# Optimization experiments

Hardware: AMD Instinct MI355X
Metric: run time of the kernel (lower is better)

## Reference

```python
import jax, jax.numpy as jnp
import numpy as np
from jax import lax

T, LC = 4096, 20           # sentence length, max word length in chars
CV, CE, CO = 100, 25, 25   # char vocab, char emb dim, char-cnn out channels
V, E = 100000, 512         # word vocab, word emb dim
H = 1024                   # lstm hidden size per direction
NT, START, STOP = 12, 10, 11
NEG = -10000.0


def _lstm_dir(x, w_ih, w_hh, b_ih, b_hh):
    # x: [T, In] -> hs: [T, H]; pytorch gate order i, f, g, o
    pre = x @ w_ih.T + (b_ih + b_hh)              # [T, 4H] (input part hoisted out of scan)
    h0 = jnp.zeros((H,), x.dtype)
    def step(carry, p):
        h, c = carry
        g = p + h @ w_hh.T
        i, f, gg, o = jnp.split(g, 4)
        i = jax.nn.sigmoid(i); f = jax.nn.sigmoid(f)
        gg = jnp.tanh(gg); o = jax.nn.sigmoid(o)
        c = f * c + i * gg
        h = o * jnp.tanh(c)
        return (h, c), h
    _, hs = lax.scan(step, (h0, h0), pre)
    return hs


def _features(sentence, chars, char_emb, cnn_w, cnn_b, word_emb,
              w_ih_f, w_hh_f, b_ih_f, b_hh_f, w_ih_b, w_hh_b, b_ih_b, b_hh_b,
              w_tag, b_tag):
    # char CNN: embed -> conv2d(kernel (3,CE), pad (2,0)) -> max-pool over full time axis
    ce = char_emb[chars][:, None, :, :]            # [T,1,LC,CE]
    y = lax.conv_general_dilated(ce, cnn_w, (1, 1), ((2, 2), (0, 0)),
                                 dimension_numbers=('NCHW', 'OIHW', 'NCHW'))
    y = y + cnn_b[None, :, None, None]             # [T,CO,LC+2,1]
    char_feat = y.max(axis=(2, 3))                 # [T,CO]
    emb = jnp.concatenate([word_emb[sentence], char_feat], axis=1)  # [T,E+CO]
    # dropout is identity in eval mode
    hf = _lstm_dir(emb, w_ih_f, w_hh_f, b_ih_f, b_hh_f)
    hb = _lstm_dir(emb[::-1], w_ih_b, w_hh_b, b_ih_b, b_hh_b)[::-1]
    out = jnp.concatenate([hf, hb], axis=1)        # [T,2H]
    return out @ w_tag.T + b_tag                   # [T,NT]


def _viterbi(feats, transitions):
    alpha0 = jnp.full((NT,), NEG, feats.dtype).at[START].set(0.0)
    def step(alpha, feat):
        smat = alpha[:, None] + feat[None, :] + transitions   # [from, to]
        return jax.nn.logsumexp(smat, axis=0), jnp.argmax(smat, axis=0)
    alpha, bptrs = lax.scan(step, alpha0, feats)               # bptrs: [T,NT]
    final = alpha + transitions[:, STOP]                       # [NT]
    score = jax.nn.logsumexp(final)
    best_last = jnp.argmax(final)
    def back(best, b):
        nb = b[best]
        return nb, nb
    _, prev = lax.scan(back, best_last, bptrs[1:][::-1])
    path = jnp.concatenate([prev[::-1], best_last[None]])      # [T]
    return score, path


def setup_inputs() -> dict:
    key = jax.random.key(0)
    ks = jax.random.split(key, 18)
    IN = E + CO
    tr = jax.random.normal(ks[17], (NT, NT), jnp.float32)
    tr = tr.at[:, START].set(NEG).at[STOP, :].set(NEG)
    return {
        'sentence': jax.random.randint(ks[0], (T,), 0, V),
        'chars': jax.random.randint(ks[1], (T, LC), 0, CV),
        'caps': jax.random.randint(ks[2], (T,), 0, 4),
        'char_emb': jax.random.normal(ks[3], (CV, CE), jnp.float32),
        'cnn_w': jax.random.normal(ks[4], (CO, 1, 3, CE), jnp.float32) * 0.1,
        'cnn_b': jax.random.normal(ks[5], (CO,), jnp.float32) * 0.1,
        'word_emb': jax.random.normal(ks[6], (V, E), jnp.float32),
        'w_ih_f': jax.random.normal(ks[7], (4 * H, IN), jnp.float32) * 0.02,
        'w_hh_f': jax.random.normal(ks[8], (4 * H, H), jnp.float32) * 0.02,
        'b_ih_f': jax.random.normal(ks[9], (4 * H,), jnp.float32) * 0.02,
        'b_hh_f': jax.random.normal(ks[10], (4 * H,), jnp.float32) * 0.02,
        'w_ih_b': jax.random.normal(ks[11], (4 * H, IN), jnp.float32) * 0.02,
        'w_hh_b': jax.random.normal(ks[12], (4 * H, H), jnp.float32) * 0.02,
        'b_ih_b': jax.random.normal(ks[13], (4 * H,), jnp.float32) * 0.02,
        'b_hh_b': jax.random.normal(ks[14], (4 * H,), jnp.float32) * 0.02,
        'w_tag': jax.random.normal(ks[15], (NT, 2 * H), jnp.float32) * 0.02,
        'b_tag': jax.random.normal(ks[16], (NT,), jnp.float32) * 0.02,
        'transitions': tr,
    }


def reference(sentence, chars, caps, char_emb, cnn_w, cnn_b, word_emb,
              w_ih_f, w_hh_f, b_ih_f, b_hh_f, w_ih_b, w_hh_b, b_ih_b, b_hh_b,
              w_tag, b_tag, transitions):
    # caps is accepted by the original forward signature but never used
    feats = _features(sentence, chars, char_emb, cnn_w, cnn_b, word_emb,
                      w_ih_f, w_hh_f, b_ih_f, b_hh_f, w_ih_b, w_hh_b,
                      b_ih_b, b_hh_b, w_tag, b_tag)
    return _viterbi(feats, transitions)
```

## Files before the change

### kernel.cpp

```cpp
#include <hip/hip_runtime.h>
#include <math.h>


#define T_LEN 4096
#define NTAG 12
#define START_TAG 10
#define STOP_TAG 11
#define NEG_VAL (-10000.0f)

typedef int   v4i __attribute__((ext_vector_type(4)));
typedef float v4f __attribute__((ext_vector_type(4)));

#define OF_EMB  0UL
#define OF_W    (OF_EMB + 4096UL * 544UL)
#define OF_BIAS (OF_W + 8192UL * 544UL)
#define OF_PRE  (OF_BIAS + 8192UL)
#define OF_HF   (OF_PRE + 4096UL * 8192UL)
#define OF_HB   (OF_HF + 4097UL * 1024UL)
#define OF_FEAT (OF_HB + 4097UL * 1024UL)

__device__ __forceinline__ float fsig(float v) {
    return 1.0f / (1.0f + __expf(-v));
}
__device__ __forceinline__ float ftanhf(float v) {
    float a = fabsf(v);
    float e = __expf(-2.0f * a);
    float r = (1.0f - e) / (1.0f + e);
    return copysignf(r, v);
}

__global__ void prep_w_kernel(const float* __restrict__ wf, const float* __restrict__ wb,
                              const float* __restrict__ bif, const float* __restrict__ bhf,
                              const float* __restrict__ bib, const float* __restrict__ bhb,
                              float* __restrict__ wpad, float* __restrict__ bias) {
    int n = blockIdx.x;
    const float* src = (n < 4096) ? (wf + (size_t)n * 537) : (wb + (size_t)(n - 4096) * 537);
    float* dst = wpad + (size_t)n * 544;
    for (int k = threadIdx.x; k < 544; k += blockDim.x)
        dst[k] = (k < 537) ? src[k] : 0.f;
    if (threadIdx.x == 0)
        bias[n] = (n < 4096) ? (bif[n] + bhf[n]) : (bib[n - 4096] + bhb[n - 4096]);
}

__global__ void charcnn_kernel(const int* __restrict__ sentence, const int* __restrict__ chars,
                               const float* __restrict__ cemb, const float* __restrict__ cw,
                               const float* __restrict__ cb, const float* __restrict__ wemb,
                               float* __restrict__ emb) {
    int t = blockIdx.x, tid = threadIdx.x;
    __shared__ float ce[500];
    __shared__ float yv[550];
    for (int i = tid; i < 500; i += 256) {
        int c = chars[t * 20 + i / 25];
        ce[i] = cemb[c * 25 + i % 25];
    }
    __syncthreads();
    for (int i = tid; i < 550; i += 256) {
        int o = i / 22, p = i % 22;
        float v = cb[o];
        #pragma unroll
        for (int kh = 0; kh < 3; ++kh) {
            int ir = p - 2 + kh;
            if (ir >= 0 && ir < 20) {
                const float* crow = ce + ir * 25;
                const float* wrow = cw + o * 75 + kh * 25;
                #pragma unroll
                for (int kw = 0; kw < 25; ++kw) v = fmaf(crow[kw], wrow[kw], v);
            }
        }
        yv[o * 22 + p] = v;
    }
    __syncthreads();
    float* erow = emb + (size_t)t * 544;
    int sidx = sentence[t];
    if (tid < 128)
        ((float4*)erow)[tid] = ((const float4*)(wemb + (size_t)sidx * 512))[tid];
    if (tid >= 128 && tid < 153) {
        int o = tid - 128;
        const float* yo = yv + o * 22;
        float m = yo[0];
        #pragma unroll
        for (int p = 1; p < 22; ++p) m = fmaxf(m, yo[p]);
        erow[512 + o] = m;
    }
    if (tid >= 160 && tid < 167) erow[537 + (tid - 160)] = 0.f;
}

__global__ __launch_bounds__(256) void sgemm_kernel(const float* __restrict__ A,
                                                    const float* __restrict__ B,
                                                    const float* __restrict__ bias,
                                                    float* __restrict__ C) {
    __shared__ float As[8 * 128];
    __shared__ float Bs[8 * 128];
    const int tid = threadIdx.x;
    const int tx = tid & 15, ty = tid >> 4;
    const int t0 = blockIdx.y * 128, n0 = blockIdx.x * 128;
    const int r = tid >> 1, cq = tid & 1;
    const int rsw = r ^ (((r >> 5) & 3) << 2);
    float acc[8][8];
    #pragma unroll
    for (int i = 0; i < 8; ++i)
        #pragma unroll
        for (int j = 0; j < 8; ++j) acc[i][j] = 0.f;
    const float* Ap = A + (size_t)(t0 + r) * 544 + cq * 4;
    const float* Bp = B + (size_t)(n0 + r) * 544 + cq * 4;
    const int bsw = ((tx >> 2) & 3) << 2;
    for (int kt = 0; kt < 68; ++kt) {
        float4 av = *(const float4*)(Ap + kt * 8);
        float4 bv = *(const float4*)(Bp + kt * 8);
        __syncthreads();
        As[(cq * 4 + 0) * 128 + r] = av.x;
        As[(cq * 4 + 1) * 128 + r] = av.y;
        As[(cq * 4 + 2) * 128 + r] = av.z;
        As[(cq * 4 + 3) * 128 + r] = av.w;
        Bs[(cq * 4 + 0) * 128 + rsw] = bv.x;
        Bs[(cq * 4 + 1) * 128 + rsw] = bv.y;
        Bs[(cq * 4 + 2) * 128 + rsw] = bv.z;
        Bs[(cq * 4 + 3) * 128 + rsw] = bv.w;
        __syncthreads();
        #pragma unroll
        for (int k = 0; k < 8; ++k) {
            float a[8], b[8];
            #pragma unroll
            for (int i = 0; i < 8; ++i) a[i] = As[k * 128 + ty * 8 + i];
            #pragma unroll
            for (int j = 0; j < 8; ++j) b[j] = Bs[k * 128 + ((tx * 8 + j) ^ bsw)];
            #pragma unroll
            for (int i = 0; i < 8; ++i)
                #pragma unroll
                for (int j = 0; j < 8; ++j) acc[i][j] = fmaf(a[i], b[j], acc[i][j]);
        }
    }
    float bz[8];
    #pragma unroll
    for (int j = 0; j < 8; ++j) bz[j] = bias[n0 + tx * 8 + j];
    #pragma unroll
    for (int i = 0; i < 8; ++i) {
        float* crow = C + (size_t)(t0 + ty * 8 + i) * 8192 + n0 + tx * 8;
        float4 s0 = make_float4(acc[i][0] + bz[0], acc[i][1] + bz[1], acc[i][2] + bz[2], acc[i][3] + bz[3]);
        float4 s1 = make_float4(acc[i][4] + bz[4], acc[i][5] + bz[5], acc[i][6] + bz[6], acc[i][7] + bz[7]);
        ((float4*)crow)[0] = s0;
        ((float4*)crow)[1] = s1;
    }
}

__global__ __launch_bounds__(512, 2) void lstm_kernel(const float* __restrict__ whhf,
                                                      const float* __restrict__ whhb,
                                                      const float* __restrict__ pre,
                                                      float* __restrict__ hfbuf,
                                                      float* __restrict__ hbbuf) {
    const int tid = threadIdx.x;
    const int dir = blockIdx.x >> 6;
    const int widx = blockIdx.x & 63;
    const int j0 = widx * 16;
    const int c32 = tid >> 4;
    const int r4 = tid & 15;
    const int lane = tid & 63;
    const int wv = tid >> 6;
    const bool pol = (r4 < 8);
    __shared__ __align__(16) float partials[2][8][64];

    v4f w[4][8];
    #pragma unroll
    for (int i = 0; i < 4; ++i) {
        int R = 4 * r4 + i;
        const v4f* wsrc = (const v4f*)((dir ? whhb : whhf) +
            (size_t)(((R >> 4) << 10) + j0 + (R & 15)) * 1024 + c32 * 32);
        #pragma unroll
        for (int m = 0; m < 8; ++m) w[i][m] = wsrc[m];
    }
    #pragma unroll
    for (int i = 0; i < 4; ++i)
        #pragma unroll
        for (int m = 0; m < 8; ++m)
            asm volatile("" : "+v"(w[i][m]));

    float* hbuf = dir ? hbbuf : hfbuf;
    const int dirofs = dir ? 4096 : 0;
    float c = 0.f;

    for (int s = 0; s < T_LEN; ++s) {
        const int t = dir ? (T_LEN - 1 - s) : s;
        const int rdslot = dir ? (t + 1) : t;
        const int wrslot = dir ? t : (t + 1);
        const int p = s & 1;

        float preg = 0.f;
        if (tid < 64)
            preg = pre[(size_t)t * 8192 + dirofs + ((lane & 3) << 10) + j0 + (lane >> 2)];

        const float* hp = hbuf + ((size_t)rdslot << 10) + c32 * 32 + r4 * 4;
        v4i hq;
        hq.x = 0; hq.y = 0; hq.z = 0; hq.w = 0;
        if (pol) {
            asm volatile("global_load_dwordx4 %0, %1, off sc1\n\ts_waitcnt vmcnt(0)"
                         : "=v"(hq) : "v"(hp));
        }
        while (true) {
            bool miss = pol && (hq.x == -1 || hq.y == -1 || hq.z == -1 || hq.w == -1);
            if (!__any(miss)) break;
            __builtin_amdgcn_s_sleep(1);
            if (miss) {
                asm volatile("global_load_dwordx4 %0, %1, off sc1\n\ts_waitcnt vmcnt(0)"
                             : "=v"(hq) : "v"(hp));
            }
        }

        float a0 = 0.f, a1 = 0.f, a2 = 0.f, a3 = 0.f;
        #pragma unroll
        for (int m = 0; m < 8; ++m) {
            int src = (lane & 48) + m;
            float hx = __shfl(__int_as_float(hq.x), src);
            float hy = __shfl(__int_as_float(hq.y), src);
            float hz = __shfl(__int_as_float(hq.z), src);
            float hw = __shfl(__int_as_float(hq.w), src);
            a0 = fmaf(w[0][m].x, hx, a0); a0 = fmaf(w[0][m].y, hy, a0);
            a0 = fmaf(w[0][m].z, hz, a0); a0 = fmaf(w[0][m].w, hw, a0);
            a1 = fmaf(w[1][m].x, hx, a1); a1 = fmaf(w[1][m].y, hy, a1);
            a1 = fmaf(w[1][m].z, hz, a1); a1 = fmaf(w[1][m].w, hw, a1);
            a2 = fmaf(w[2][m].x, hx, a2); a2 = fmaf(w[2][m].y, hy, a2);
            a2 = fmaf(w[2][m].z, hz, a2); a2 = fmaf(w[2][m].w, hw, a2);
            a3 = fmaf(w[3][m].x, hx, a3); a3 = fmaf(w[3][m].y, hy, a3);
            a3 = fmaf(w[3][m].z, hz, a3); a3 = fmaf(w[3][m].w, hw, a3);
        }
        a0 += __shfl_xor(a0, 16); a0 += __shfl_xor(a0, 32);
        a1 += __shfl_xor(a1, 16); a1 += __shfl_xor(a1, 32);
        a2 += __shfl_xor(a2, 16); a2 += __shfl_xor(a2, 32);
        a3 += __shfl_xor(a3, 16); a3 += __shfl_xor(a3, 32);
        if ((lane >> 4) == 0)
            *(float4*)&partials[p][wv][r4 << 2] = make_float4(a0, a1, a2, a3);
        __syncthreads();

        if (tid < 64) {
            int rql = ((lane & 3) << 4) + (lane >> 2);
            float dsum = 0.f;
            #pragma unroll
            for (int q = 0; q < 8; ++q) dsum += partials[p][q][rql];
            float val = preg + dsum;
            float act = ((lane & 3) == 2) ? ftanhf(val) : fsig(val);
            int base = lane & ~3;
            float iv = __shfl(act, base);
            float fv = __shfl(act, base + 1);
            float gv = __shfl(act, base + 2);
            float ov = __shfl(act, base + 3);
            c = fv * c + iv * gv;
            float h = ov * ftanhf(c);
            v4f hv;
            hv.x = __shfl(h, (lane << 4) & 63);
            hv.y = __shfl(h, ((lane << 4) + 4) & 63);
            hv.z = __shfl(h, ((lane << 4) + 8) & 63);
            hv.w = __shfl(h, ((lane << 4) + 12) & 63);
            if (lane < 4) {
                float* hp2 = hbuf + ((size_t)wrslot << 10) + j0 + (lane << 2);
                asm volatile("global_store_dwordx4 %0, %1, off sc1"
                             :: "v"(hp2), "v"(hv));
            }
        }
    }
}

__global__ __launch_bounds__(192) void tagproj_kernel(const float* __restrict__ hfbuf,
                                                      const float* __restrict__ hbbuf,
                                                      const float* __restrict__ wtag,
                                                      const float* __restrict__ btag,
                                                      float* __restrict__ feats) {
    int t = blockIdx.x, tid = threadIdx.x;
    __shared__ float4 hs4[512];
    for (int i = tid; i < 512; i += 192) {
        float4 q = (i < 256)
            ? ((const float4*)(hfbuf + ((size_t)(t + 1) << 10)))[i]
            : ((const float4*)(hbbuf + ((size_t)t << 10)))[i - 256];
        hs4[i ^ ((i >> 5) & 7)] = q;
    }
    __syncthreads();
    int tag = tid >> 4, sl = tid & 15;
    const float4* wrow4 = (const float4*)(wtag + (size_t)tag * 2048 + (sl << 7));
    float a = 0.f;
    #pragma unroll
    for (int m = 0; m < 32; ++m) {
        float4 h4 = hs4[(sl << 5) + (m ^ (sl & 7))];
        float4 w4 = wrow4[m];
        a = fmaf(h4.x, w4.x, a);
        a = fmaf(h4.y, w4.y, a);
        a = fmaf(h4.z, w4.z, a);
        a = fmaf(h4.w, w4.w, a);
    }
    a += __shfl_xor(a, 1);
    a += __shfl_xor(a, 2);
    a += __shfl_xor(a, 4);
    a += __shfl_xor(a, 8);
    if (sl == 0) feats[t * 12 + tag] = a + btag[tag];
}

__global__ __launch_bounds__(64) void viterbi_kernel(const float* __restrict__ feats,
                                                     const float* __restrict__ trans,
                                                     float* __restrict__ out) {
    const int tid = threadIdx.x;
    __shared__ float fbuf[256 * 12];
    __shared__ unsigned char bp[4096 * 12];
    __shared__ __align__(16) float alph[12];
    __shared__ __align__(16) float finv[12];
    float trf[12];
    float tstop = 0.f;
    if (tid < 12) {
        #pragma unroll
        for (int f = 0; f < 12; ++f) trf[f] = trans[f * 12 + tid];
        tstop = trans[tid * 12 + STOP_TAG];
        alph[tid] = (tid == START_TAG) ? 0.f : NEG_VAL;
    }
    __syncthreads();
    for (int ck = 0; ck < 16; ++ck) {
        for (int i = tid; i < 3072; i += 64) fbuf[i] = feats[ck * 3072 + i];
        __syncthreads();
        for (int tt = 0; tt < 256; ++tt) {
            if (tid < 12) {
                float feat = fbuf[tt * 12 + tid];
                float4 A0 = *(const float4*)(alph);
                float4 A1 = *(const float4*)(alph + 4);
                float4 A2 = *(const float4*)(alph + 8);
                float av[12] = {A0.x, A0.y, A0.z, A0.w, A1.x, A1.y, A1.z, A1.w,
                                A2.x, A2.y, A2.z, A2.w};
                float sv[12];
                float m = -INFINITY;
                int best = 0;
                #pragma unroll
                for (int f = 0; f < 12; ++f) {
                    float s2 = (av[f] + feat) + trf[f];
                    sv[f] = s2;
                    if (s2 > m) { m = s2; best = f; }
                }
                float sum = 0.f;
                #pragma unroll
                for (int f = 0; f < 12; ++f) sum += __expf(sv[f] - m);
                bp[(ck * 256 + tt) * 12 + tid] = (unsigned char)best;
                alph[tid] = __logf(sum) + m;
            }
            __syncthreads();
        }
    }
    if (tid < 12) finv[tid] = alph[tid] + tstop;
    __syncthreads();
    if (tid < 12) {
        float4 F0 = *(const float4*)(finv);
        float4 F1 = *(const float4*)(finv + 4);
        float4 F2 = *(const float4*)(finv + 8);
        float fv[12] = {F0.x, F0.y, F0.z, F0.w, F1.x, F1.y, F1.z, F1.w,
                        F2.x, F2.y, F2.z, F2.w};
        float m = -INFINITY;
        int bl = 0;
        #pragma unroll
        for (int f = 0; f < 12; ++f)
            if (fv[f] > m) { m = fv[f]; bl = f; }
        float sum = 0.f;
        #pragma unroll
        for (int f = 0; f < 12; ++f) sum += __expf(fv[f] - m);
        float score = __logf(sum) + m;
        if (tid == 0) {
            out[0] = score;
            out[4096] = (float)bl;
        }
        int cur = bl;
        for (int tt = 4095; tt >= 1; --tt) {
            int bv = (int)bp[tt * 12 + tid];
            cur = __shfl(bv, cur);
            if (tid == 0) out[tt] = (float)cur;
        }
    }
}

extern "C" void kernel_launch(void* const* d_in, const int* in_sizes, int n_in,
                              void* d_out, int out_size, void* d_ws, size_t ws_size,
                              hipStream_t stream) {
    (void)in_sizes; (void)n_in; (void)out_size; (void)ws_size;
    const int* sentence = (const int*)d_in[0];
    const int* chars = (const int*)d_in[1];
    const float* cemb = (const float*)d_in[3];
    const float* cw = (const float*)d_in[4];
    const float* cb = (const float*)d_in[5];
    const float* wemb = (const float*)d_in[6];
    const float* w_ih_f = (const float*)d_in[7];
    const float* w_hh_f = (const float*)d_in[8];
    const float* b_ih_f = (const float*)d_in[9];
    const float* b_hh_f = (const float*)d_in[10];
    const float* w_ih_b = (const float*)d_in[11];
    const float* w_hh_b = (const float*)d_in[12];
    const float* b_ih_b = (const float*)d_in[13];
    const float* b_hh_b = (const float*)d_in[14];
    const float* wtag = (const float*)d_in[15];
    const float* btag = (const float*)d_in[16];
    const float* trans = (const float*)d_in[17];

    float* ws = (float*)d_ws;
    float* emb = ws + OF_EMB;
    float* wpad = ws + OF_W;
    float* bias = ws + OF_BIAS;
    float* pre = ws + OF_PRE;
    float* hf = ws + OF_HF;
    float* hb = ws + OF_HB;
    float* feats = ws + OF_FEAT;

    (void)hipMemsetAsync(hf, 0xFF, 4097UL * 1024UL * 4UL, stream);
    (void)hipMemsetAsync(hb, 0xFF, 4097UL * 1024UL * 4UL, stream);
    (void)hipMemsetAsync(hf, 0x00, 1024UL * 4UL, stream);
    (void)hipMemsetAsync(hb + 4096UL * 1024UL, 0x00, 1024UL * 4UL, stream);

    hipLaunchKernelGGL(prep_w_kernel, dim3(8192), dim3(256), 0, stream,
                       w_ih_f, w_ih_b, b_ih_f, b_hh_f, b_ih_b, b_hh_b, wpad, bias);
    hipLaunchKernelGGL(charcnn_kernel, dim3(4096), dim3(256), 0, stream,
                       sentence, chars, cemb, cw, cb, wemb, emb);
    hipLaunchKernelGGL(sgemm_kernel, dim3(64, 32), dim3(256), 0, stream,
                       emb, wpad, bias, pre);
    hipLaunchKernelGGL(lstm_kernel, dim3(128), dim3(512), 0, stream,
                       w_hh_f, w_hh_b, pre, hf, hb);
    hipLaunchKernelGGL(tagproj_kernel, dim3(4096), dim3(192), 0, stream,
                       hf, hb, wtag, btag, feats);
    hipLaunchKernelGGL(viterbi_kernel, dim3(1), dim3(64), 0, stream,
                       feats, trans, (float*)d_out);
}
```

Measured before the change: 11.46 ms.

## Use bf16 MFMA for input projection GEMM and register-shuffle Viterbi

Converts the word/char embeddings and input-to-hidden weights to bf16 and replaces the FP32 SIMT GEMM with a bf16 MFMA 16x16x32 kernel that accumulates in FP32. Separately, the Viterbi forward pass keeps alpha in registers and exchanges it with wavefront shuffles, removing the per-step block barrier and shared-memory round trips. The bf16 inputs lower the precision of the pre-activations, which feed a long recurrence and an argmax decode, so the path output could diverge from the reference.

```diff
diff --git a/kernel.cpp b/kernel.cpp
--- a/kernel.cpp
+++ b/kernel.cpp
@@ -10,6 +10,8 @@
 
 typedef int   v4i __attribute__((ext_vector_type(4)));
 typedef float v4f __attribute__((ext_vector_type(4)));
+typedef short sh8 __attribute__((ext_vector_type(8)));
+typedef float f32x4 __attribute__((ext_vector_type(4)));
 
 #define OF_EMB  0UL
 #define OF_W    (OF_EMB + 4096UL * 544UL)
@@ -28,16 +30,21 @@
     float r = (1.0f - e) / (1.0f + e);
     return copysignf(r, v);
 }
+__device__ __forceinline__ unsigned f2bf(float x) {
+    unsigned u = __float_as_uint(x);
+    u += 0x7fffu + ((u >> 16) & 1u);
+    return u >> 16;
+}
 
 __global__ void prep_w_kernel(const float* __restrict__ wf, const float* __restrict__ wb,
                               const float* __restrict__ bif, const float* __restrict__ bhf,
                               const float* __restrict__ bib, const float* __restrict__ bhb,
-                              float* __restrict__ wpad, float* __restrict__ bias) {
+                              unsigned short* __restrict__ wbf, float* __restrict__ bias) {
     int n = blockIdx.x;
     const float* src = (n < 4096) ? (wf + (size_t)n * 537) : (wb + (size_t)(n - 4096) * 537);
-    float* dst = wpad + (size_t)n * 544;
+    unsigned short* dst = wbf + (size_t)n * 544;
     for (int k = threadIdx.x; k < 544; k += blockDim.x)
-        dst[k] = (k < 537) ? src[k] : 0.f;
+        dst[k] = (k < 537) ? (unsigned short)f2bf(src[k]) : (unsigned short)0;
     if (threadIdx.x == 0)
         bias[n] = (n < 4096) ? (bif[n] + bhf[n]) : (bib[n - 4096] + bhb[n - 4096]);
 }
@@ -45,7 +52,7 @@
 __global__ void charcnn_kernel(const int* __restrict__ sentence, const int* __restrict__ chars,
                                const float* __restrict__ cemb, const float* __restrict__ cw,
                                const float* __restrict__ cb, const float* __restrict__ wemb,
-                               float* __restrict__ emb) {
+                               unsigned short* __restrict__ emb) {
     int t = blockIdx.x, tid = threadIdx.x;
     __shared__ float ce[500];
     __shared__ float yv[550];
@@ -70,76 +77,80 @@
         yv[o * 22 + p] = v;
     }
     __syncthreads();
-    float* erow = emb + (size_t)t * 544;
+    unsigned short* erow = emb + (size_t)t * 544;
     int sidx = sentence[t];
-    if (tid < 128)
-        ((float4*)erow)[tid] = ((const float4*)(wemb + (size_t)sidx * 512))[tid];
+    if (tid < 128) {
+        float4 v = ((const float4*)(wemb + (size_t)sidx * 512))[tid];
+        uint2 pk;
+        pk.x = f2bf(v.x) | (f2bf(v.y) << 16);
+        pk.y = f2bf(v.z) | (f2bf(v.w) << 16);
+        ((uint2*)erow)[tid] = pk;
+    }
     if (tid >= 128 && tid < 153) {
         int o = tid - 128;
         const float* yo = yv + o * 22;
         float m = yo[0];
         #pragma unroll
         for (int p = 1; p < 22; ++p) m = fmaxf(m, yo[p]);
-        erow[512 + o] = m;
-    }
-    if (tid >= 160 && tid < 167) erow[537 + (tid - 160)] = 0.f;
-}
-
-__global__ __launch_bounds__(256) void sgemm_kernel(const float* __restrict__ A,
-                                                    const float* __restrict__ B,
+        erow[512 + o] = (unsigned short)f2bf(m);
+    }
+    if (tid >= 160 && tid < 167) erow[537 + (tid - 160)] = 0;
+}
+
+__global__ __launch_bounds__(256) void sgemm_kernel(const unsigned short* __restrict__ A,
+                                                    const unsigned short* __restrict__ B,
                                                     const float* __restrict__ bias,
                                                     float* __restrict__ C) {
-    __shared__ float As[8 * 128];
-    __shared__ float Bs[8 * 128];
+    __shared__ unsigned short As[128 * 40];
+    __shared__ unsigned short Bs[128 * 40];
     const int tid = threadIdx.x;
-    const int tx = tid & 15, ty = tid >> 4;
-    const int t0 = blockIdx.y * 128, n0 = blockIdx.x * 128;
-    const int r = tid >> 1, cq = tid & 1;
-    const int rsw = r ^ (((r >> 5) & 3) << 2);
-    float acc[8][8];
+    const int wv = tid >> 6, lane = tid & 63;
+    const int l15 = lane & 15, l4 = lane >> 4;
+    const int m0 = blockIdx.y * 128, n0 = blockIdx.x * 128;
+    const int srow = tid >> 2, sslot = tid & 3;
+
+    f32x4 acc[2][8];
     #pragma unroll
-    for (int i = 0; i < 8; ++i)
-        #pragma unroll
-        for (int j = 0; j < 8; ++j) acc[i][j] = 0.f;
-    const float* Ap = A + (size_t)(t0 + r) * 544 + cq * 4;
-    const float* Bp = B + (size_t)(n0 + r) * 544 + cq * 4;
-    const int bsw = ((tx >> 2) & 3) << 2;
-    for (int kt = 0; kt < 68; ++kt) {
-        float4 av = *(const float4*)(Ap + kt * 8);
-        float4 bv = *(const float4*)(Bp + kt * 8);
+    for (int mt = 0; mt < 2; ++mt)
+        #pragma unroll
+        for (int nt = 0; nt < 8; ++nt) acc[mt][nt] = (f32x4){0.f, 0.f, 0.f, 0.f};
+
+    for (int kt = 0; kt < 17; ++kt) {
+        const int kof = kt * 32 + sslot * 8;
+        uint4 a0 = *(const uint4*)(A + (size_t)(m0 + srow) * 544 + kof);
+        uint4 a1 = *(const uint4*)(A + (size_t)(m0 + 64 + srow) * 544 + kof);
+        uint4 b0 = *(const uint4*)(B + (size_t)(n0 + srow) * 544 + kof);
+        uint4 b1 = *(const uint4*)(B + (size_t)(n0 + 64 + srow) * 544 + kof);
         __syncthreads();
-        As[(cq * 4 + 0) * 128 + r] = av.x;
-        As[(cq * 4 + 1) * 128 + r] = av.y;
-        As[(cq * 4 + 2) * 128 + r] = av.z;
-        As[(cq * 4 + 3) * 128 + r] = av.w;
-        Bs[(cq * 4 + 0) * 128 + rsw] = bv.x;
-        Bs[(cq * 4 + 1) * 128 + rsw] = bv.y;
-        Bs[(cq * 4 + 2) * 128 + rsw] = bv.z;
-        Bs[(cq * 4 + 3) * 128 + rsw] = bv.w;
+        *(uint4*)&As[srow * 40 + sslot * 8] = a0;
+        *(uint4*)&As[(64 + srow) * 40 + sslot * 8] = a1;
+        *(uint4*)&Bs[srow * 40 + sslot * 8] = b0;
+        *(uint4*)&Bs[(64 + srow) * 40 + sslot * 8] = b1;
         __syncthreads();
-        #pragma unroll
-        for (int k = 0; k < 8; ++k) {
-            float a[8], b[8];
+        sh8 bfr[8];
+        #pragma unroll
+        for (int nt = 0; nt < 8; ++nt)
+            bfr[nt] = *(const sh8*)&Bs[(16 * nt + l15) * 40 + l4 * 8];
+        #pragma unroll
+        for (int mt = 0; mt < 2; ++mt) {
+            sh8 afr = *(const sh8*)&As[(32 * wv + 16 * mt + l15) * 40 + l4 * 8];
             #pragma unroll
-            for (int i = 0; i < 8; ++i) a[i] = As[k * 128 + ty * 8 + i];
+            for (int nt = 0; nt < 8; ++nt)
+                acc[mt][nt] = __builtin_amdgcn_mfma_f32_16x16x32_bf16(
+                    afr, bfr[nt], acc[mt][nt], 0, 0, 0);
+        }
+    }
+    #pragma unroll
+    for (int mt = 0; mt < 2; ++mt) {
+        int mrow = m0 + 32 * wv + 16 * mt + l4 * 4;
+        #pragma unroll
+        for (int nt = 0; nt < 8; ++nt) {
+            int col = n0 + 16 * nt + l15;
+            float bz = bias[col];
             #pragma unroll
-            for (int j = 0; j < 8; ++j) b[j] = Bs[k * 128 + ((tx * 8 + j) ^ bsw)];
-            #pragma unroll
-            for (int i = 0; i < 8; ++i)
-                #pragma unroll
-                for (int j = 0; j < 8; ++j) acc[i][j] = fmaf(a[i], b[j], acc[i][j]);
-        }
-    }
-    float bz[8];
-    #pragma unroll
-    for (int j = 0; j < 8; ++j) bz[j] = bias[n0 + tx * 8 + j];
-    #pragma unroll
-    for (int i = 0; i < 8; ++i) {
-        float* crow = C + (size_t)(t0 + ty * 8 + i) * 8192 + n0 + tx * 8;
-        float4 s0 = make_float4(acc[i][0] + bz[0], acc[i][1] + bz[1], acc[i][2] + bz[2], acc[i][3] + bz[3]);
-        float4 s1 = make_float4(acc[i][4] + bz[4], acc[i][5] + bz[5], acc[i][6] + bz[6], acc[i][7] + bz[7]);
-        ((float4*)crow)[0] = s0;
-        ((float4*)crow)[1] = s1;
+            for (int r = 0; r < 4; ++r)
+                C[(size_t)(mrow + r) * 8192 + col] = acc[mt][nt][r] + bz;
+        }
     }
 }
 
@@ -297,62 +308,55 @@
     const int tid = threadIdx.x;
     __shared__ float fbuf[256 * 12];
     __shared__ unsigned char bp[4096 * 12];
-    __shared__ __align__(16) float alph[12];
-    __shared__ __align__(16) float finv[12];
     float trf[12];
+    float alpha = NEG_VAL;
     float tstop = 0.f;
     if (tid < 12) {
         #pragma unroll
         for (int f = 0; f < 12; ++f) trf[f] = trans[f * 12 + tid];
+        if (tid == START_TAG) alpha = 0.f;
         tstop = trans[tid * 12 + STOP_TAG];
-        alph[tid] = (tid == START_TAG) ? 0.f : NEG_VAL;
-    }
-    __syncthreads();
+    }
     for (int ck = 0; ck < 16; ++ck) {
+        __syncthreads();
         for (int i = tid; i < 3072; i += 64) fbuf[i] = feats[ck * 3072 + i];
         __syncthreads();
-        for (int tt = 0; tt < 256; ++tt) {
-            if (tid < 12) {
+        if (tid < 12) {
+            for (int tt = 0; tt < 256; ++tt) {
                 float feat = fbuf[tt * 12 + tid];
-                float4 A0 = *(const float4*)(alph);
-                float4 A1 = *(const float4*)(alph + 4);
-                float4 A2 = *(const float4*)(alph + 8);
-                float av[12] = {A0.x, A0.y, A0.z, A0.w, A1.x, A1.y, A1.z, A1.w,
-                                A2.x, A2.y, A2.z, A2.w};
                 float sv[12];
                 float m = -INFINITY;
                 int best = 0;
                 #pragma unroll
                 for (int f = 0; f < 12; ++f) {
-                    float s2 = (av[f] + feat) + trf[f];
-                    sv[f] = s2;
-                    if (s2 > m) { m = s2; best = f; }
+                    float af = __shfl(alpha, f);
+                    float s = (af + feat) + trf[f];
+                    sv[f] = s;
+                    if (s > m) { m = s; best = f; }
                 }
                 float sum = 0.f;
                 #pragma unroll
                 for (int f = 0; f < 12; ++f) sum += __expf(sv[f] - m);
+                alpha = __logf(sum) + m;
                 bp[(ck * 256 + tt) * 12 + tid] = (unsigned char)best;
-                alph[tid] = __logf(sum) + m;
             }
-            __syncthreads();
-        }
-    }
-    if (tid < 12) finv[tid] = alph[tid] + tstop;
-    __syncthreads();
+        }
+    }
     if (tid < 12) {
-        float4 F0 = *(const float4*)(finv);
-        float4 F1 = *(const float4*)(finv + 4);
-        float4 F2 = *(const float4*)(finv + 8);
-        float fv[12] = {F0.x, F0.y, F0.z, F0.w, F1.x, F1.y, F1.z, F1.w,
-                        F2.x, F2.y, F2.z, F2.w};
+        float fin = alpha + tstop;
         float m = -INFINITY;
         int bl = 0;
         #pragma unroll
-        for (int f = 0; f < 12; ++f)
-            if (fv[f] > m) { m = fv[f]; bl = f; }
+        for (int f = 0; f < 12; ++f) {
+            float vf = __shfl(fin, f);
+            if (vf > m) { m = vf; bl = f; }
+        }
         float sum = 0.f;
         #pragma unroll
-        for (int f = 0; f < 12; ++f) sum += __expf(fv[f] - m);
+        for (int f = 0; f < 12; ++f) {
+            float vf = __shfl(fin, f);
+            sum += __expf(vf - m);
+        }
         float score = __logf(sum) + m;
         if (tid == 0) {
             out[0] = score;
@@ -390,8 +394,8 @@
     const float* trans = (const float*)d_in[17];
 
     float* ws = (float*)d_ws;
-    float* emb = ws + OF_EMB;
-    float* wpad = ws + OF_W;
+    unsigned short* emb_bf = (unsigned short*)(ws + OF_EMB);
+    unsigned short* w_bf = (unsigned short*)(ws + OF_W);
     float* bias = ws + OF_BIAS;
     float* pre = ws + OF_PRE;
     float* hf = ws + OF_HF;
@@ -404,11 +408,11 @@
     (void)hipMemsetAsync(hb + 4096UL * 1024UL, 0x00, 1024UL * 4UL, stream);
 
     hipLaunchKernelGGL(prep_w_kernel, dim3(8192), dim3(256), 0, stream,
-                       w_ih_f, w_ih_b, b_ih_f, b_hh_f, b_ih_b, b_hh_b, wpad, bias);
+                       w_ih_f, w_ih_b, b_ih_f, b_hh_f, b_ih_b, b_hh_b, w_bf, bias);
     hipLaunchKernelGGL(charcnn_kernel, dim3(4096), dim3(256), 0, stream,
-                       sentence, chars, cemb, cw, cb, wemb, emb);
+                       sentence, chars, cemb, cw, cb, wemb, emb_bf);
     hipLaunchKernelGGL(sgemm_kernel, dim3(64, 32), dim3(256), 0, stream,
-                       emb, wpad, bias, pre);
+                       emb_bf, w_bf, bias, pre);
     hipLaunchKernelGGL(lstm_kernel, dim3(128), dim3(512), 0, stream,
                        w_hh_f, w_hh_b, pre, hf, hb);
     hipLaunchKernelGGL(tagproj_kernel, dim3(4096), dim3(192), 0, stream,
```

Result: faster. 11.09 ms (-3.3%).
